# Kernel optimization log

Hardware: AMD Instinct MI355X
Metric: run time of the kernel (lower is better)

## Reference

```python
import jax, jax.numpy as jnp
import numpy as np

N_NODES = 50000
N_EDGES = 800000
NODE_IN_DIM = 768
NODE_DIM = 512
OUTPUT_NUM = 97
B, P = 8, 2048


def setup_inputs() -> dict:
    key = jax.random.key(0)
    ks = jax.random.split(key, 10)
    node_features = jax.random.normal(ks[0], (N_NODES, NODE_IN_DIM), jnp.float32)
    edge_features = jax.random.normal(ks[1], (N_EDGES, 32), jnp.float32)
    src = jax.random.randint(ks[2], (N_EDGES,), 0, N_NODES)
    dst = jax.random.randint(ks[3], (N_EDGES,), 0, N_NODES)
    head_ent_nodes = jax.random.randint(ks[4], (B, P), 0, N_NODES)
    tail_ent_nodes = jax.random.randint(ks[5], (B, P), 0, N_NODES)
    # params (xavier-ish scale for weights)
    W1 = jax.random.normal(ks[6], (NODE_IN_DIM, NODE_DIM), jnp.float32) / np.sqrt(NODE_IN_DIM)
    b1 = jax.random.normal(ks[7], (NODE_DIM,), jnp.float32) * 0.01
    Wp = jax.random.normal(ks[8], (2 * NODE_DIM, OUTPUT_NUM), jnp.float32) / np.sqrt(2 * NODE_DIM)
    bp = jax.random.normal(ks[9], (OUTPUT_NUM,), jnp.float32) * 0.01
    return {
        "node_features": node_features, "edge_features": edge_features,
        "W1": W1, "b1": b1, "Wp": Wp, "bp": bp,
        "src": src, "dst": dst,
        "head_ent_nodes": head_ent_nodes, "tail_ent_nodes": tail_ent_nodes,
    }


def reference(node_features, edge_features, W1, b1, Wp, bp, src, dst, head_ent_nodes, tail_ent_nodes):
    n = node_features.shape[0]
    # node_fc: Linear + ReLU
    h = jax.nn.relu(node_features @ W1 + b1)  # [N, D]
    # DGL update_all: message = dst node's own h, mean-reduced at dst.
    # (src is part of the graph but unused by this message function.)
    msg = h[dst]  # [E, D] gather
    agg = jax.ops.segment_sum(msg, dst, num_segments=n)  # [N, D]
    deg = jax.ops.segment_sum(jnp.ones((dst.shape[0],), h.dtype), dst, num_segments=n)  # [N]
    # nodes with no incoming messages keep their old h (DGL UDF semantics)
    h_new = jnp.where((deg > 0)[:, None], agg / jnp.maximum(deg, 1.0)[:, None], h)
    head = h_new[head_ent_nodes]  # [B, P, D]
    tail = h_new[tail_ent_nodes]  # [B, P, D]
    out = jnp.concatenate([head, tail], axis=2) @ Wp + bp  # [B, P, 97]
    return out
```

## Files before the change

### kernel.cpp

```cpp
#include <hip/hip_runtime.h>
#include <hip/hip_bf16.h>
#include <stdint.h>

using bf16x8 = __attribute__((ext_vector_type(8))) short;
using f32x4  = __attribute__((ext_vector_type(4))) float;

#define N_NODES  50000
#define K1       768
#define D1       512
#define NPAIR    16384
#define NOUT     97
#define NOUT_PAD 112
#define MTILES   391
#define NTILES   4
#define NWG      (MTILES * NTILES)
#define WGPX     196

__device__ __forceinline__ uint16_t f2bf(float f) {
    uint32_t u = __builtin_bit_cast(uint32_t, f);
    return (uint16_t)((u + 0x7fffu + ((u >> 16) & 1u)) >> 16);
}

__device__ __forceinline__ uint32_t cvt_pk_bf16(float lo, float hi) {
    uint32_t r;
    asm("v_cvt_pk_bf16_f32 %0, %1, %2" : "=v"(r) : "v"(lo), "v"(hi));
    return r;
}

__device__ __forceinline__ void gll16(const void* g, void* l) {
    __builtin_amdgcn_global_load_lds(
        (const __attribute__((address_space(1))) void*)g,
        (__attribute__((address_space(3))) void*)l, 16, 0, 0);
}

__global__ void k_convert(const float* __restrict__ W1, const float* __restrict__ Wp,
                          uint16_t* __restrict__ W1t, uint16_t* __restrict__ Wpt) {
    int idx = blockIdx.x * 256 + threadIdx.x;
    const int n1 = D1 * K1;
    if (idx < n1) {
        int c = idx / K1, k = idx - c * K1;
        W1t[idx] = f2bf(W1[k * D1 + c]);
    } else {
        int j = idx - n1;
        if (j < NOUT_PAD * 1024) {
            int c = j >> 10, k = j & 1023;
            Wpt[j] = (c < NOUT) ? f2bf(Wp[k * NOUT + c]) : (uint16_t)0;
        }
    }
}

__global__ __launch_bounds__(256) void k_gemm1(const float* __restrict__ A,
        const uint16_t* __restrict__ W1t, const float* __restrict__ bias1,
        uint16_t* __restrict__ H) {
    __shared__ float    lds_a[4096];
    __shared__ uint16_t lds_b[4096];

    const int bid = blockIdx.x;
    const int tt = (bid & 7) * WGPX + (bid >> 3);
    if (tt >= NWG) return;
    const int m0 = (tt >> 2) * 128, n0 = (tt & 3) * 128;

    const int t = threadIdx.x, lane = t & 63, w = t >> 6;
    const int wm = w >> 1, wn = w & 1;
    const int cl = lane & 15, kh = lane >> 4;
    const int l3 = lane >> 3, l7 = lane & 7;

    const float* aSrc[4];
    #pragma unroll
    for (int i = 0; i < 4; ++i) {
        int r = m0 + w * 32 + i * 8 + l3;
        if (r >= N_NODES) r = N_NODES - 1;
        aSrc[i] = A + (size_t)r * K1 + ((l7 ^ (l3 & 7)) * 4);
    }
    const uint16_t* bSrc[2];
    #pragma unroll
    for (int i = 0; i < 2; ++i)
        bSrc[i] = W1t + (size_t)(n0 + w * 32 + i * 16 + (lane >> 2)) * K1 + (lane & 3) * 8;

    float*    aDst = &lds_a[w * 1024];
    uint16_t* bDst = &lds_b[w * 1024];

    const int q = lane & 7;
    const int pa0 = ((2 * kh) ^ q) * 4, pa1 = ((2 * kh + 1) ^ q) * 4;
    const int arow0 = (wm * 64 + cl) * 32;
    const int brow0 = (wn * 64 + cl) * 32 + kh * 8;

    f32x4 acc[4][4];
    const f32x4 z = {0.f, 0.f, 0.f, 0.f};
    #pragma unroll
    for (int m = 0; m < 4; ++m)
        #pragma unroll
        for (int n = 0; n < 4; ++n) acc[m][n] = z;

    for (int kt = 0; kt < K1 / 32; ++kt) {
        #pragma unroll
        for (int i = 0; i < 4; ++i) gll16(aSrc[i], aDst + i * 256);
        #pragma unroll
        for (int i = 0; i < 2; ++i) gll16(bSrc[i], bDst + i * 512);
        #pragma unroll
        for (int i = 0; i < 4; ++i) aSrc[i] += 32;
        #pragma unroll
        for (int i = 0; i < 2; ++i) bSrc[i] += 32;
        __syncthreads();

        bf16x8 af[4], bfr[4];
        #pragma unroll
        for (int m = 0; m < 4; ++m) {
            f32x4 r0 = *(const f32x4*)&lds_a[arow0 + m * 512 + pa0];
            f32x4 r1 = *(const f32x4*)&lds_a[arow0 + m * 512 + pa1];
            uint32_t uu[4];
            uu[0] = cvt_pk_bf16(r0[0], r0[1]);
            uu[1] = cvt_pk_bf16(r0[2], r0[3]);
            uu[2] = cvt_pk_bf16(r1[0], r1[1]);
            uu[3] = cvt_pk_bf16(r1[2], r1[3]);
            af[m] = *(const bf16x8*)uu;
        }
        #pragma unroll
        for (int n = 0; n < 4; ++n)
            bfr[n] = *(const bf16x8*)&lds_b[brow0 + n * 512];
        #pragma unroll
        for (int m = 0; m < 4; ++m)
            #pragma unroll
            for (int n = 0; n < 4; ++n)
                acc[m][n] = __builtin_amdgcn_mfma_f32_16x16x32_bf16(af[m], bfr[n], acc[m][n], 0, 0, 0);
        __syncthreads();
    }

    float bv[4]; int bcol[4];
    #pragma unroll
    for (int n = 0; n < 4; ++n) { bcol[n] = n0 + wn * 64 + n * 16 + cl; bv[n] = bias1[bcol[n]]; }
    #pragma unroll
    for (int m = 0; m < 4; ++m) {
        int rbase = m0 + wm * 64 + m * 16 + kh * 4;
        #pragma unroll
        for (int rr = 0; rr < 4; ++rr) {
            int row = rbase + rr;
            if (row < N_NODES) {
                #pragma unroll
                for (int n = 0; n < 4; ++n) {
                    float v = acc[m][n][rr] + bv[n];
                    H[(size_t)row * D1 + bcol[n]] = f2bf(fmaxf(v, 0.f));
                }
            }
        }
    }
}

__global__ __launch_bounds__(256) void k_gemm2(const uint16_t* __restrict__ H,
        const uint16_t* __restrict__ Wpt, const float* __restrict__ bp,
        const int* __restrict__ head, const int* __restrict__ tail,
        float* __restrict__ out) {
    __shared__ uint16_t lds_w[NOUT_PAD][40];
    const int t = threadIdx.x;
    const int lane = t & 63, wave = t >> 6;
    const int cl = lane & 15, kh = lane >> 4;
    const int rowbase = blockIdx.x * 64 + wave * 16;
    const int i_l = rowbase + cl;
    const int nodeH = head[i_l], nodeT = tail[i_l];
    const uint16_t* hH = H + (size_t)nodeH * D1 + kh * 8;
    const uint16_t* hT = H + (size_t)nodeT * D1 + kh * 8;

    f32x4 acc[7];
    const f32x4 z = {0.f, 0.f, 0.f, 0.f};
    #pragma unroll
    for (int n = 0; n < 7; ++n) acc[n] = z;

    const int wrow = t >> 1, whalf = t & 1;
    const uint16_t* wsrc = Wpt + (size_t)wrow * 1024 + whalf * 16;
    uint16_t* wdst = &lds_w[wrow][whalf * 16];

    for (int kb = 0; kb < 32; ++kb) {
        uint4 w0 = {0,0,0,0}, w1 = {0,0,0,0};
        if (t < 224) {
            const uint4* wp4 = (const uint4*)(wsrc + kb * 32);
            w0 = wp4[0]; w1 = wp4[1];
        }
        bf16x8 af = (kb < 16) ? *(const bf16x8*)(hH + kb * 32)
                              : *(const bf16x8*)(hT + (kb - 16) * 32);
        __syncthreads();
        if (t < 224) { ((uint4*)wdst)[0] = w0; ((uint4*)wdst)[1] = w1; }
        __syncthreads();
        #pragma unroll
        for (int n = 0; n < 7; ++n) {
            bf16x8 bfr = *(const bf16x8*)&lds_w[n * 16 + cl][kh * 8];
            acc[n] = __builtin_amdgcn_mfma_f32_16x16x32_bf16(af, bfr, acc[n], 0, 0, 0);
        }
    }
    #pragma unroll
    for (int n = 0; n < 7; ++n) {
        int col = n * 16 + cl;
        if (col < NOUT) {
            float bb = bp[col];
            #pragma unroll
            for (int rr = 0; rr < 4; ++rr) {
                int i = rowbase + kh * 4 + rr;
                out[(size_t)i * NOUT + col] = acc[n][rr] + bb;
            }
        }
    }
}

extern "C" void kernel_launch(void* const* d_in, const int* in_sizes, int n_in,
                              void* d_out, int out_size, void* d_ws, size_t ws_size,
                              hipStream_t stream) {
    const float* node_features = (const float*)d_in[0];
    const float* W1   = (const float*)d_in[2];
    const float* b1   = (const float*)d_in[3];
    const float* Wp   = (const float*)d_in[4];
    const float* bp   = (const float*)d_in[5];
    const int* head   = (const int*)d_in[8];
    const int* tail   = (const int*)d_in[9];
    float* out = (float*)d_out;

    char* ws = (char*)d_ws;
    uint16_t* H   = (uint16_t*)ws;
    uint16_t* W1t = (uint16_t*)(ws + (size_t)N_NODES * D1 * 2);
    uint16_t* Wpt = (uint16_t*)(ws + (size_t)N_NODES * D1 * 2 + (size_t)D1 * K1 * 2);

    const int convN = D1 * K1 + NOUT_PAD * 1024;
    k_convert<<<(convN + 255) / 256, 256, 0, stream>>>(W1, Wp, W1t, Wpt);

    k_gemm1<<<WGPX * 8, 256, 0, stream>>>(node_features, W1t, b1, H);

    k_gemm2<<<NPAIR / 64, 256, 0, stream>>>(H, Wpt, bp, head, tail, out);
}
```

Baseline: 105.6 us.

## Double-buffer LDS in GEMM1 with async prefetch and fix bank-conflict swizzles

Doubles the LDS buffers for the node-feature GEMM so the global-to-LDS loads for the next K step are issued before computing the current one. A partial vmcnt wait lets loads overlap with MFMA work instead of stalling on each tile. It also changes the XOR swizzle on the A and B LDS layouts to reduce bank conflicts on fragment reads. LDS use per block doubles, which may lower occupancy, and the manual waitcnt/barrier sequence is fragile.

```diff
diff --git a/kernel.cpp b/kernel.cpp
--- a/kernel.cpp
+++ b/kernel.cpp
@@ -15,6 +15,7 @@
 #define NTILES   4
 #define NWG      (MTILES * NTILES)
 #define WGPX     196
+#define KSTEPS   (K1 / 32)
 
 __device__ __forceinline__ uint16_t f2bf(float f) {
     uint32_t u = __builtin_bit_cast(uint32_t, f);
@@ -52,8 +53,8 @@
 __global__ __launch_bounds__(256) void k_gemm1(const float* __restrict__ A,
         const uint16_t* __restrict__ W1t, const float* __restrict__ bias1,
         uint16_t* __restrict__ H) {
-    __shared__ float    lds_a[4096];
-    __shared__ uint16_t lds_b[4096];
+    __shared__ float    lds_a[2 * 4096];
+    __shared__ uint16_t lds_b[2 * 4096];
 
     const int bid = blockIdx.x;
     const int tt = (bid & 7) * WGPX + (bid >> 3);
@@ -70,20 +71,21 @@
     for (int i = 0; i < 4; ++i) {
         int r = m0 + w * 32 + i * 8 + l3;
         if (r >= N_NODES) r = N_NODES - 1;
-        aSrc[i] = A + (size_t)r * K1 + ((l7 ^ (l3 & 7)) * 4);
+        aSrc[i] = A + (size_t)r * K1 + ((l7 ^ l3) * 4);
     }
     const uint16_t* bSrc[2];
     #pragma unroll
     for (int i = 0; i < 2; ++i)
-        bSrc[i] = W1t + (size_t)(n0 + w * 32 + i * 16 + (lane >> 2)) * K1 + (lane & 3) * 8;
+        bSrc[i] = W1t + (size_t)(n0 + w * 32 + i * 16 + (lane >> 2)) * K1
+                      + (((lane & 3) ^ ((lane >> 3) & 3)) * 8);
 
     float*    aDst = &lds_a[w * 1024];
     uint16_t* bDst = &lds_b[w * 1024];
 
-    const int q = lane & 7;
-    const int pa0 = ((2 * kh) ^ q) * 4, pa1 = ((2 * kh + 1) ^ q) * 4;
+    const int q7 = cl & 7;
+    const int pa0 = ((2 * kh) ^ q7) * 4, pa1 = ((2 * kh + 1) ^ q7) * 4;
     const int arow0 = (wm * 64 + cl) * 32;
-    const int brow0 = (wn * 64 + cl) * 32 + kh * 8;
+    const int brow0 = (wn * 64 + cl) * 32 + ((kh ^ ((cl >> 1) & 3)) * 8);
 
     f32x4 acc[4][4];
     const f32x4 z = {0.f, 0.f, 0.f, 0.f};
@@ -92,39 +94,58 @@
         #pragma unroll
         for (int n = 0; n < 4; ++n) acc[m][n] = z;
 
-    for (int kt = 0; kt < K1 / 32; ++kt) {
-        #pragma unroll
-        for (int i = 0; i < 4; ++i) gll16(aSrc[i], aDst + i * 256);
-        #pragma unroll
-        for (int i = 0; i < 2; ++i) gll16(bSrc[i], bDst + i * 512);
-        #pragma unroll
-        for (int i = 0; i < 4; ++i) aSrc[i] += 32;
-        #pragma unroll
-        for (int i = 0; i < 2; ++i) bSrc[i] += 32;
-        __syncthreads();
-
-        bf16x8 af[4], bfr[4];
-        #pragma unroll
-        for (int m = 0; m < 4; ++m) {
-            f32x4 r0 = *(const f32x4*)&lds_a[arow0 + m * 512 + pa0];
-            f32x4 r1 = *(const f32x4*)&lds_a[arow0 + m * 512 + pa1];
-            uint32_t uu[4];
-            uu[0] = cvt_pk_bf16(r0[0], r0[1]);
-            uu[1] = cvt_pk_bf16(r0[2], r0[3]);
-            uu[2] = cvt_pk_bf16(r1[0], r1[1]);
-            uu[3] = cvt_pk_bf16(r1[2], r1[3]);
-            af[m] = *(const bf16x8*)uu;
-        }
-        #pragma unroll
-        for (int n = 0; n < 4; ++n)
-            bfr[n] = *(const bf16x8*)&lds_b[brow0 + n * 512];
-        #pragma unroll
-        for (int m = 0; m < 4; ++m)
-            #pragma unroll
-            for (int n = 0; n < 4; ++n)
-                acc[m][n] = __builtin_amdgcn_mfma_f32_16x16x32_bf16(af[m], bfr[n], acc[m][n], 0, 0, 0);
-        __syncthreads();
-    }
+#define STAGE(BUF) do {                                                    \
+    _Pragma("unroll")                                                      \
+    for (int i = 0; i < 4; ++i) gll16(aSrc[i], aDst + (BUF) * 4096 + i * 256); \
+    _Pragma("unroll")                                                      \
+    for (int i = 0; i < 2; ++i) gll16(bSrc[i], bDst + (BUF) * 4096 + i * 512); \
+    _Pragma("unroll")                                                      \
+    for (int i = 0; i < 4; ++i) aSrc[i] += 32;                             \
+    _Pragma("unroll")                                                      \
+    for (int i = 0; i < 2; ++i) bSrc[i] += 32;                             \
+    } while (0)
+
+#define COMPUTE(BUF) do {                                                  \
+    const float*    la = &lds_a[(BUF) * 4096];                             \
+    const uint16_t* lb = &lds_b[(BUF) * 4096];                             \
+    bf16x8 af[4], bfr[4];                                                  \
+    _Pragma("unroll")                                                      \
+    for (int n = 0; n < 4; ++n)                                            \
+        bfr[n] = *(const bf16x8*)&lb[brow0 + n * 512];                     \
+    _Pragma("unroll")                                                      \
+    for (int m = 0; m < 4; ++m) {                                          \
+        f32x4 r0 = *(const f32x4*)&la[arow0 + m * 512 + pa0];              \
+        f32x4 r1 = *(const f32x4*)&la[arow0 + m * 512 + pa1];              \
+        uint32_t uu[4];                                                    \
+        uu[0] = cvt_pk_bf16(r0[0], r0[1]);                                 \
+        uu[1] = cvt_pk_bf16(r0[2], r0[3]);                                 \
+        uu[2] = cvt_pk_bf16(r1[0], r1[1]);                                 \
+        uu[3] = cvt_pk_bf16(r1[2], r1[3]);                                 \
+        af[m] = *(const bf16x8*)uu;                                        \
+    }                                                                      \
+    _Pragma("unroll")                                                      \
+    for (int m = 0; m < 4; ++m)                                            \
+        _Pragma("unroll")                                                  \
+        for (int n = 0; n < 4; ++n)                                        \
+            acc[m][n] = __builtin_amdgcn_mfma_f32_16x16x32_bf16(           \
+                            af[m], bfr[n], acc[m][n], 0, 0, 0);            \
+    } while (0)
+
+    STAGE(0);
+    for (int kt = 0; kt < KSTEPS - 1; ++kt) {
+        const int cur = kt & 1;
+        STAGE(cur ^ 1);
+        asm volatile("s_waitcnt vmcnt(6)" ::: "memory");
+        __builtin_amdgcn_s_barrier();
+        COMPUTE(cur);
+        __builtin_amdgcn_s_barrier();
+    }
+    asm volatile("s_waitcnt vmcnt(0)" ::: "memory");
+    __builtin_amdgcn_s_barrier();
+    COMPUTE((KSTEPS - 1) & 1);
+
+#undef STAGE
+#undef COMPUTE
 
     float bv[4]; int bcol[4];
     #pragma unroll
```

New measurement: 109.9 us. +4.0%, slower.
